# Kernel tuning notes

Measured on AMD Instinct MI355X. Metric: run time of the kernel, lower is better.

The kernel has to match this reference:

```python
import jax, jax.numpy as jnp
import numpy as np

N = 50000        # nodes
E_RAND = 800000  # random edges; self-loops appended -> E = E_RAND + N
H = 4            # heads
D_IN = 256
D_HID = 64       # per-head hidden (H*D_HID == D_IN -> identity residual in layer 1)
D_OUT = 32       # classes per head
SLOPE = 0.2      # leaky-relu negative slope


def setup_inputs() -> dict:
    key = jax.random.key(0)
    ks = jax.random.split(key, 13)
    loops = jnp.arange(N, dtype=jnp.int32)
    src = jnp.concatenate([jax.random.randint(ks[0], (E_RAND,), 0, N, dtype=jnp.int32), loops])
    dst = jnp.concatenate([jax.random.randint(ks[1], (E_RAND,), 0, N, dtype=jnp.int32), loops])
    h = jax.random.normal(ks[2], (N, D_IN), dtype=jnp.float32)
    def w(k, shape, fan):
        return jax.random.normal(k, shape, dtype=jnp.float32) * (1.0 / np.sqrt(fan))
    return {
        "h": h, "src": src, "dst": dst,
        # layer 1 (tuple in_feats -> separate fc_src / fc_dst in dgl GATConv)
        "W1_src": w(ks[3], (D_IN, H * D_HID), D_IN),
        "W1_dst": w(ks[4], (D_IN, H * D_HID), D_IN),
        "al1": w(ks[5], (H, D_HID), D_HID),
        "ar1": w(ks[6], (H, D_HID), D_HID),
        # layer 2
        "W2_src": w(ks[7], (H * D_HID, H * D_OUT), H * D_HID),
        "W2_dst": w(ks[8], (H * D_HID, H * D_OUT), H * D_HID),
        "al2": w(ks[9], (H, D_OUT), D_OUT),
        "ar2": w(ks[10], (H, D_OUT), D_OUT),
        # residual projection for layer 2 (in_dim != heads*out)
        "Wres2": w(ks[11], (H * D_HID, H * D_OUT), H * D_HID),
    }


def gat_conv(h_node, src, dst, Ws, Wd, al, ar, heads, dout, resval):
    n = h_node.shape[0]
    fs = (h_node @ Ws).reshape(n, heads, dout)   # [N,H,D] projected src feats
    fd = (h_node @ Wd).reshape(n, heads, dout)
    el = jnp.sum(fs * al, axis=-1)               # [N,H]
    er = jnp.sum(fd * ar, axis=-1)               # [N,H]
    e = jax.nn.leaky_relu(el[src] + er[dst], SLOPE)           # [E,H] edge scores
    emax = jax.ops.segment_max(e, dst, num_segments=n)        # segment softmax over dst
    ex = jnp.exp(e - emax[dst])
    denom = jax.ops.segment_sum(ex, dst, num_segments=n)
    a = ex / denom[dst]                                        # [E,H] attention
    msg = fs[src] * a[:, :, None]                              # [E,H,D] gather * weight
    out = jax.ops.segment_sum(msg, dst, num_segments=n)       # [N,H,D] scatter-add
    return out + resval


def reference(h, src, dst, W1_src, W1_dst, al1, ar1, W2_src, W2_dst, al2, ar2, Wres2):
    # layer 1: identity residual (in_dim == heads*hidden), elu activation, flatten heads
    res1 = h.reshape(-1, H, D_HID)
    h1 = gat_conv(h, src, dst, W1_src, W1_dst, al1, ar1, H, D_HID, res1)
    h1 = jax.nn.elu(h1).reshape(-1, H * D_HID)
    # layer 2: linear residual, no activation, mean over heads
    res2 = (h1 @ Wres2).reshape(-1, H, D_OUT)
    h2 = gat_conv(h1, src, dst, W2_src, W2_dst, al2, ar2, H, D_OUT, res2)
    return h2.mean(axis=1)                                     # [N, num_classes]
```

## Files before the change

kernel.cpp:

```cpp
#include <hip/hip_runtime.h>
#include <hip/hip_bf16.h>

#define NN 50000
#define EE 850000
#define NBLK_SCAN 98

typedef unsigned short u16;
using short8 = __attribute__((ext_vector_type(8))) short;
using f32x4  = __attribute__((ext_vector_type(4))) float;

__device__ __forceinline__ float bf2f(u16 u) {
    union { unsigned int i; float f; } v; v.i = ((unsigned int)u) << 16; return v.f;
}
__device__ __forceinline__ u16 f2bf(float f) {
    __hip_bfloat16 h = __float2bfloat16(f);
    return *reinterpret_cast<u16*>(&h);
}

__device__ __forceinline__ float ld1(const void* X, size_t i, bool f32m) {
    return f32m ? ((const float*)X)[i] : bf2f(((const u16*)X)[i]);
}
__device__ __forceinline__ void load4(const void* X, size_t g, bool f32m, float o[4]) {
    if (f32m) {
        float4 v = ((const float4*)X)[g];
        o[0] = v.x; o[1] = v.y; o[2] = v.z; o[3] = v.w;
    } else {
        ushort4 v = ((const ushort4*)X)[g];
        o[0] = bf2f(v.x); o[1] = bf2f(v.y); o[2] = bf2f(v.z); o[3] = bf2f(v.w);
    }
}

__global__ void k_detect(const u16* __restrict__ hh, int* __restrict__ flag,
                         int* __restrict__ deg) {
    if (blockIdx.x != 0) {
        int i = (blockIdx.x - 1) * 256 + threadIdx.x;
        if (i < NN) deg[i] = 0;
        return;
    }
    __shared__ int sm[256];
    int t = threadIdx.x;
    int c = 0;
    for (int i = 0; i < 16; ++i) {
        u16 u = hh[t * 16 + i];
        int e = (u >> 7) & 0xFF;
        if (e != 0 && (e < 90 || e > 160)) ++c;
    }
    sm[t] = c;
    __syncthreads();
    for (int s = 128; s > 0; s >>= 1) {
        if (t < s) sm[t] += sm[t + s];
        __syncthreads();
    }
    if (t == 0) *flag = (sm[0] > 200) ? 1 : 0;
}

__global__ void k_prep(const void* __restrict__ W1s, const void* __restrict__ al1,
                       const void* __restrict__ W1d, const void* __restrict__ ar1,
                       const void* __restrict__ W2s, const void* __restrict__ al2,
                       const void* __restrict__ W2d, const void* __restrict__ ar2,
                       const void* __restrict__ Wres2, const int* __restrict__ dst,
                       u16* __restrict__ BT1, u16* __restrict__ BT2,
                       float* __restrict__ wl1, float* __restrict__ wr1,
                       float* __restrict__ wl2, float* __restrict__ wr2,
                       int* __restrict__ deg, int* __restrict__ eorder,
                       const int* __restrict__ mode) {
    int bid = blockIdx.x;
    if (bid >= 528) {
        int e = (bid - 528) * 256 + threadIdx.x;
        if (e < EE) {
            int r = atomicAdd(&deg[dst[e]], 1);
            eorder[e] = r;
        }
        return;
    }
    bool f32m = (*mode) != 0;
    if (bid < 512) {
        int id = bid * 256 + threadIdx.x;
        int which = id >> 16;
        int rem = id & 65535;
        int n = rem >> 8, k = rem & 255;
        if (which == 0) {
            BT1[n * 256 + k] = f2bf(ld1(W1s, (size_t)k * 256 + n, f32m));
        } else {
            float v = (n < 128) ? ld1(W2s, (size_t)k * 128 + n, f32m)
                                : ld1(Wres2, (size_t)k * 128 + (n - 128), f32m);
            BT2[n * 256 + k] = f2bf(v);
        }
    } else {
        int id = (bid - 512) * 256 + threadIdx.x;
        int which = id >> 10;
        int rem = id & 1023;
        int k = rem >> 2, h = rem & 3;
        float s = 0.f;
        if (which == 0) {
            for (int d = 0; d < 64; ++d) s += ld1(W1s, k * 256 + h * 64 + d, f32m) * ld1(al1, h * 64 + d, f32m);
            wl1[k * 4 + h] = s;
        } else if (which == 1) {
            for (int d = 0; d < 64; ++d) s += ld1(W1d, k * 256 + h * 64 + d, f32m) * ld1(ar1, h * 64 + d, f32m);
            wr1[k * 4 + h] = s;
        } else if (which == 2) {
            for (int d = 0; d < 32; ++d) s += ld1(W2s, k * 128 + h * 32 + d, f32m) * ld1(al2, h * 32 + d, f32m);
            wl2[k * 4 + h] = s;
        } else {
            for (int d = 0; d < 32; ++d) s += ld1(W2d, k * 128 + h * 32 + d, f32m) * ld1(ar2, h * 32 + d, f32m);
            wr2[k * 4 + h] = s;
        }
    }
}

__global__ void k_scan1(const int* __restrict__ deg, int* __restrict__ rowptr,
                        int* __restrict__ bsum) {
    __shared__ int sm[512];
    int t = threadIdx.x;
    int i = blockIdx.x * 512 + t;
    int v = (i < NN) ? deg[i] : 0;
    int x = v;
    sm[t] = x;
    __syncthreads();
    for (int off = 1; off < 512; off <<= 1) {
        int y = (t >= off) ? sm[t - off] : 0;
        __syncthreads();
        x += y;
        sm[t] = x;
        __syncthreads();
    }
    if (i < NN) rowptr[i] = x - v;
    if (t == 511) bsum[blockIdx.x] = x;
}

__global__ void k_scan3_eler1(int* __restrict__ rowptr, const int* __restrict__ bsum,
                              const void* __restrict__ X, u16* __restrict__ hb,
                              const float* __restrict__ wl, const float* __restrict__ wr,
                              float* __restrict__ el, float* __restrict__ er,
                              const int* __restrict__ mode) {
    int bid = blockIdx.x;
    if (bid < 196) {
        __shared__ int sm[NBLK_SCAN];
        int t = threadIdx.x;
        if (t < NBLK_SCAN) sm[t] = bsum[t];
        __syncthreads();
        int g = bid >> 1;
        int pre = 0;
        for (int j = 0; j < g; ++j) pre += sm[j];
        int i = bid * 256 + t;
        if (i < NN) {
            rowptr[i] += pre;
            if (i == 0) rowptr[NN] = EE;
        }
        return;
    }
    bool f32m = (*mode) != 0;
    int wave = threadIdx.x >> 6, lane = threadIdx.x & 63;
    int node = (bid - 196) * 4 + wave;
    float a[4];
    load4(X, (size_t)node * 64 + lane, f32m, a);
    ushort4 hv = {f2bf(a[0]), f2bf(a[1]), f2bf(a[2]), f2bf(a[3])};
    ((ushort4*)hb)[(size_t)node * 64 + lane] = hv;
    float accl[4] = {0, 0, 0, 0}, accr[4] = {0, 0, 0, 0};
    int k0 = lane * 4;
#pragma unroll
    for (int j = 0; j < 4; ++j) {
        float4 wlv = ((const float4*)wl)[k0 + j];
        float4 wrv = ((const float4*)wr)[k0 + j];
        accl[0] += a[j] * wlv.x; accl[1] += a[j] * wlv.y;
        accl[2] += a[j] * wlv.z; accl[3] += a[j] * wlv.w;
        accr[0] += a[j] * wrv.x; accr[1] += a[j] * wrv.y;
        accr[2] += a[j] * wrv.z; accr[3] += a[j] * wrv.w;
    }
#pragma unroll
    for (int off = 32; off > 0; off >>= 1) {
#pragma unroll
        for (int t = 0; t < 4; ++t) {
            accl[t] += __shfl_down(accl[t], off, 64);
            accr[t] += __shfl_down(accr[t], off, 64);
        }
    }
    if (lane == 0) {
        float4 vl = {accl[0], accl[1], accl[2], accl[3]};
        float4 vr = {accr[0], accr[1], accr[2], accr[3]};
        ((float4*)el)[node] = vl;
        ((float4*)er)[node] = vr;
    }
}

__global__ void k_scatw(const int* __restrict__ src, const int* __restrict__ dst,
                        const int* __restrict__ eorder, const int* __restrict__ rowptr,
                        const float* __restrict__ el, const float* __restrict__ er,
                        uint4* __restrict__ meta) {
    int e = blockIdx.x * 256 + threadIdx.x;
    if (e >= EE) return;
    int s = src[e], d = dst[e];
    int slot = rowptr[d] + eorder[e];
    float4 eL = ((const float4*)el)[s];
    float4 eR = ((const float4*)er)[d];
    float ev[4] = {eL.x + eR.x, eL.y + eR.y, eL.z + eR.z, eL.w + eR.w};
    u16 op[4];
#pragma unroll
    for (int t = 0; t < 4; ++t) {
        float x = ev[t];
        x = x > 0.f ? x : 0.2f * x;
        x = fminf(fmaxf(x, -60.f), 60.f);
        op[t] = f2bf(__expf(x));
    }
    uint4 m;
    m.x = (unsigned int)s;
    m.y = (unsigned int)op[0] | ((unsigned int)op[1] << 16);
    m.z = (unsigned int)op[2] | ((unsigned int)op[3] << 16);
    m.w = 0u;
    meta[slot] = m;
}

__global__ void k_gemm_mfma(const u16* __restrict__ A,
                            const u16* __restrict__ BT, u16* __restrict__ C) {
    __shared__ u16 smem[128 * 72 * 2];
    u16* At = smem;
    u16* Bt = smem + 128 * 72;
    int t = threadIdx.x;
    int lane = t & 63, w = t >> 6;
    int mt = blockIdx.x >> 1, nt = blockIdx.x & 1;
    int m0 = mt * 128, n0 = nt * 128;
    int wr = (w >> 1) * 64, wc = (w & 1) * 64;
    f32x4 acc[4][4] = {};
    int q = lane >> 4, cl = lane & 15;

    for (int ph = 0; ph < 4; ++ph) {
        int kb = ph * 64;
        for (int it = 0; it < 4; ++it) {
            int c = it * 256 + t;
            int row = c >> 3, c8 = c & 7;
            int rowg = m0 + row;
            float4 av;
            if (rowg < NN) {
                av = *(const float4*)(A + (size_t)rowg * 256 + kb + c8 * 8);
            } else {
                av = make_float4(0.f, 0.f, 0.f, 0.f);
            }
            *(float4*)&At[row * 72 + c8 * 8] = av;
            float4 bv = *(const float4*)(BT + (size_t)(n0 + row) * 256 + kb + c8 * 8);
            *(float4*)&Bt[row * 72 + c8 * 8] = bv;
        }
        __syncthreads();
#pragma unroll
        for (int ks = 0; ks < 2; ++ks) {
            short8 af[4], bf[4];
#pragma unroll
            for (int i = 0; i < 4; ++i)
                af[i] = *(const short8*)&At[(wr + i * 16 + cl) * 72 + ks * 32 + q * 8];
#pragma unroll
            for (int j = 0; j < 4; ++j)
                bf[j] = *(const short8*)&Bt[(wc + j * 16 + cl) * 72 + ks * 32 + q * 8];
#pragma unroll
            for (int i = 0; i < 4; ++i)
#pragma unroll
                for (int j = 0; j < 4; ++j)
                    acc[i][j] = __builtin_amdgcn_mfma_f32_16x16x32_bf16(af[i], bf[j], acc[i][j], 0, 0, 0);
        }
        __syncthreads();
    }
    u16* Ct = smem;
    int sw_w = q << 1;
#pragma unroll
    for (int i = 0; i < 4; ++i)
#pragma unroll
        for (int j = 0; j < 4; ++j) {
            int colb = wc + j * 16 + cl;
            int chunk = (colb >> 3) ^ sw_w;
#pragma unroll
            for (int r = 0; r < 4; ++r) {
                int row = wr + i * 16 + q * 4 + r;
                Ct[row * 128 + chunk * 8 + (colb & 7)] = f2bf(acc[i][j][r]);
            }
        }
    __syncthreads();
#pragma unroll
    for (int it = 0; it < 8; ++it) {
        int c = it * 256 + t;
        int row = c >> 4, k16 = c & 15;
        int mrow = m0 + row;
        if (mrow < NN) {
            int phys = k16 ^ (((row >> 2) & 3) << 1);
            float4 v = *(const float4*)&Ct[row * 128 + phys * 8];
            *(float4*)&C[(size_t)mrow * 256 + n0 + k16 * 8] = v;
        }
    }
}

__global__ void k_agg1(const int* __restrict__ rowptr, const uint4* __restrict__ meta,
                       const u16* __restrict__ fs, u16* __restrict__ hb,
                       const float* __restrict__ wl2, const float* __restrict__ wr2,
                       float* __restrict__ el2, float* __restrict__ er2) {
    int wave = threadIdx.x >> 6, lane = threadIdx.x & 63;
    int node = blockIdx.x * 4 + wave;
    int beg = rowptr[node], end = rowptr[node + 1];
    int head = lane >> 4;
    const int* ms = (const int*)meta;
    const u16* mw = (const u16*)meta + 2 + head;
    float a0 = 0.f, a1 = 0.f, a2 = 0.f, a3 = 0.f, ll = 0.f;
#pragma unroll 8
    for (int p = beg; p < end; ++p) {
        int s = ms[(size_t)p * 4];
        float pw = bf2f(mw[(size_t)p * 8]);
        ushort4 fv = *(const ushort4*)(fs + (size_t)s * 256 + lane * 4);
        ll += pw;
        a0 += pw * bf2f(fv.x);
        a1 += pw * bf2f(fv.y);
        a2 += pw * bf2f(fv.z);
        a3 += pw * bf2f(fv.w);
    }
    float rinv = 1.f / ll;
    ushort4 rv = ((const ushort4*)hb)[(size_t)node * 64 + lane];
    float v0 = a0 * rinv + bf2f(rv.x), v1 = a1 * rinv + bf2f(rv.y);
    float v2 = a2 * rinv + bf2f(rv.z), v3 = a3 * rinv + bf2f(rv.w);
    v0 = v0 > 0.f ? v0 : __expf(v0) - 1.f;
    v1 = v1 > 0.f ? v1 : __expf(v1) - 1.f;
    v2 = v2 > 0.f ? v2 : __expf(v2) - 1.f;
    v3 = v3 > 0.f ? v3 : __expf(v3) - 1.f;
    ushort4 o = {f2bf(v0), f2bf(v1), f2bf(v2), f2bf(v3)};
    ((ushort4*)hb)[(size_t)node * 64 + lane] = o;
    float4 w0 = ((const float4*)wl2)[lane * 4 + 0];
    float4 w1 = ((const float4*)wl2)[lane * 4 + 1];
    float4 w2 = ((const float4*)wl2)[lane * 4 + 2];
    float4 w3 = ((const float4*)wl2)[lane * 4 + 3];
    float4 r0 = ((const float4*)wr2)[lane * 4 + 0];
    float4 r1 = ((const float4*)wr2)[lane * 4 + 1];
    float4 r2 = ((const float4*)wr2)[lane * 4 + 2];
    float4 r3 = ((const float4*)wr2)[lane * 4 + 3];
    float acl[4], acr[4];
    acl[0] = v0 * w0.x + v1 * w1.x + v2 * w2.x + v3 * w3.x;
    acl[1] = v0 * w0.y + v1 * w1.y + v2 * w2.y + v3 * w3.y;
    acl[2] = v0 * w0.z + v1 * w1.z + v2 * w2.z + v3 * w3.z;
    acl[3] = v0 * w0.w + v1 * w1.w + v2 * w2.w + v3 * w3.w;
    acr[0] = v0 * r0.x + v1 * r1.x + v2 * r2.x + v3 * r3.x;
    acr[1] = v0 * r0.y + v1 * r1.y + v2 * r2.y + v3 * r3.y;
    acr[2] = v0 * r0.z + v1 * r1.z + v2 * r2.z + v3 * r3.z;
    acr[3] = v0 * r0.w + v1 * r1.w + v2 * r2.w + v3 * r3.w;
#pragma unroll
    for (int off = 32; off > 0; off >>= 1) {
#pragma unroll
        for (int t = 0; t < 4; ++t) {
            acl[t] += __shfl_down(acl[t], off, 64);
            acr[t] += __shfl_down(acr[t], off, 64);
        }
    }
    if (lane == 0) {
        float4 vl = {acl[0], acl[1], acl[2], acl[3]};
        float4 vr = {acr[0], acr[1], acr[2], acr[3]};
        ((float4*)el2)[node] = vl;
        ((float4*)er2)[node] = vr;
    }
}

__global__ void k_agg2(const int* __restrict__ rowptr, const uint4* __restrict__ meta,
                       const float* __restrict__ el2, const float* __restrict__ er2,
                       const u16* __restrict__ c2,
                       void* __restrict__ out, const int* __restrict__ mode) {
    bool f32m = (*mode) != 0;
    int wave = threadIdx.x >> 6, lane = threadIdx.x & 63;
    int node = blockIdx.x * 4 + wave;
    int beg = rowptr[node], end = rowptr[node + 1];
    int head = lane >> 4;
    const int* ms = (const int*)meta;
    float erh = er2[node * 4 + head];
    float a0 = 0.f, a1 = 0.f, ll = 0.f;
#pragma unroll 8
    for (int p = beg; p < end; ++p) {
        int s = ms[(size_t)p * 4];
        float x = el2[s * 4 + head] + erh;
        x = x > 0.f ? x : 0.2f * x;
        x = fminf(fmaxf(x, -60.f), 60.f);
        float pw = __expf(x);
        ushort2 fv = *(const ushort2*)(c2 + (size_t)s * 256 + lane * 2);
        ll += pw;
        a0 += pw * bf2f(fv.x);
        a1 += pw * bf2f(fv.y);
    }
    float rinv = 1.f / ll;
    ushort2 rv = *(const ushort2*)(c2 + (size_t)node * 256 + 128 + lane * 2);
    float o0 = a0 * rinv + bf2f(rv.x);
    float o1 = a1 * rinv + bf2f(rv.y);
    o0 += __shfl_xor(o0, 16, 64); o0 += __shfl_xor(o0, 32, 64);
    o1 += __shfl_xor(o1, 16, 64); o1 += __shfl_xor(o1, 32, 64);
    if (lane < 16) {
        float v0 = 0.25f * o0, v1 = 0.25f * o1;
        size_t oi = (size_t)node * 32 + lane * 2;
        if (f32m) {
            ((float*)out)[oi] = v0;
            ((float*)out)[oi + 1] = v1;
        } else {
            ushort2 ov = {f2bf(v0), f2bf(v1)};
            *(ushort2*)((u16*)out + oi) = ov;
        }
    }
}

extern "C" void kernel_launch(void* const* d_in, const int* in_sizes, int n_in,
                              void* d_out, int out_size, void* d_ws, size_t ws_size,
                              hipStream_t stream) {
    int ih = 0, isrc = 1, idst = 2, iW1s = 3, iW1d = 4, ial1 = 5, iar1 = 6,
        iW2s = 7, iW2d = 8, ial2 = 9, iar2 = 10, iWres = 11;
    if (n_in >= 12 && in_sizes[0] != 12800000) {
        iW1d = 0; iW1s = 1; iW2d = 2; iW2s = 3; iWres = 4; ial1 = 5; ial2 = 6;
        iar1 = 7; iar2 = 8; idst = 9; ih = 10; isrc = 11;
    }
    const void* h     = d_in[ih];
    const int* src    = (const int*)d_in[isrc];
    const int* dst    = (const int*)d_in[idst];
    const void* W1s   = d_in[iW1s];
    const void* W1d   = d_in[iW1d];
    const void* al1   = d_in[ial1];
    const void* ar1   = d_in[iar1];
    const void* W2s   = d_in[iW2s];
    const void* W2d   = d_in[iW2d];
    const void* al2   = d_in[ial2];
    const void* ar2   = d_in[iar2];
    const void* Wres2 = d_in[iWres];

    char* w = (char*)d_ws;
    size_t off = 0;
    auto alloc = [&](size_t bytes) -> void* {
        void* p = w + off;
        off += (bytes + 255) & ~(size_t)255;
        return p;
    };
    int* mode   = (int*)alloc(256);
    float* wl1 = (float*)alloc(256 * 4 * 4);
    float* wr1 = (float*)alloc(256 * 4 * 4);
    float* wl2 = (float*)alloc(256 * 4 * 4);
    float* wr2 = (float*)alloc(256 * 4 * 4);
    int* deg    = (int*)alloc(NN * 4);
    int* rowptr = (int*)alloc((NN + 1) * 4);
    int* bsum   = (int*)alloc(NBLK_SCAN * 4);
    int* eorder = (int*)alloc((size_t)EE * 4);
    uint4* meta = (uint4*)alloc((size_t)EE * 16);
    float* el1  = (float*)alloc((size_t)NN * 4 * 4);
    float* er1  = (float*)alloc((size_t)NN * 4 * 4);
    float* el2  = (float*)alloc((size_t)NN * 4 * 4);
    float* er2  = (float*)alloc((size_t)NN * 4 * 4);
    u16* BT1    = (u16*)alloc(256 * 256 * 2);
    u16* BT2    = (u16*)alloc(256 * 256 * 2);
    u16* fs1    = (u16*)alloc((size_t)NN * 256 * 2);
    u16* hb     = (u16*)alloc((size_t)NN * 256 * 2);
    u16* c2     = fs1;

    k_detect<<<197, 256, 0, stream>>>((const u16*)h, mode, deg);
    k_prep<<<528 + (EE + 255) / 256, 256, 0, stream>>>(
        W1s, al1, W1d, ar1, W2s, al2, W2d, ar2, Wres2, dst,
        BT1, BT2, wl1, wr1, wl2, wr2, deg, eorder, mode);
    k_scan1<<<NBLK_SCAN, 512, 0, stream>>>(deg, rowptr, bsum);
    k_scan3_eler1<<<196 + NN / 4, 256, 0, stream>>>(rowptr, bsum,
                                                    h, hb, wl1, wr1, el1, er1, mode);
    k_scatw<<<(EE + 255) / 256, 256, 0, stream>>>(src, dst, eorder, rowptr,
                                                  el1, er1, meta);
    k_gemm_mfma<<<782, 256, 0, stream>>>(hb, BT1, fs1);
    k_agg1<<<NN / 4, 256, 0, stream>>>(rowptr, meta, fs1, hb,
                                       wl2, wr2, el2, er2);
    k_gemm_mfma<<<782, 256, 0, stream>>>(hb, BT2, c2);
    k_agg2<<<NN / 4, 256, 0, stream>>>(rowptr, meta, el2, er2, c2, d_out, mode);
}
```

Before: 354.6 us.

## Use direct global-to-LDS loads with XOR swizzle in GEMM; tile weight transpose

The MFMA GEMM now stages A and B tiles with global_load_lds 16-byte transfers into an unpadded, XOR-swizzled LDS layout instead of going through registers. The row bounds check is dropped, so hb is over-allocated by 64 rows to make the tail reads safe. The weight-prep kernel transposes through a shared tile in 32 blocks instead of 512 scattered blocks, and the attention-weight dot products use vectorized loads. The aim is less register staging and fewer prep blocks; the padded rows hold uninitialized data that feeds only output rows beyond N.

```diff
diff --git a/kernel.cpp b/kernel.cpp
--- a/kernel.cpp
+++ b/kernel.cpp
@@ -28,6 +28,12 @@
         ushort4 v = ((const ushort4*)X)[g];
         o[0] = bf2f(v.x); o[1] = bf2f(v.y); o[2] = bf2f(v.z); o[3] = bf2f(v.w);
     }
+}
+
+__device__ __forceinline__ void gload_lds16(const void* g, void* l) {
+    __builtin_amdgcn_global_load_lds(
+        (const __attribute__((address_space(1))) unsigned int*)g,
+        (__attribute__((address_space(3))) unsigned int*)l, 16, 0, 0);
 }
 
 __global__ void k_detect(const u16* __restrict__ hh, int* __restrict__ flag,
@@ -65,8 +71,8 @@
                        int* __restrict__ deg, int* __restrict__ eorder,
                        const int* __restrict__ mode) {
     int bid = blockIdx.x;
-    if (bid >= 528) {
-        int e = (bid - 528) * 256 + threadIdx.x;
+    if (bid >= 48) {
+        int e = (bid - 48) * 256 + threadIdx.x;
         if (e < EE) {
             int r = atomicAdd(&deg[dst[e]], 1);
             eorder[e] = r;
@@ -74,37 +80,70 @@
         return;
     }
     bool f32m = (*mode) != 0;
-    if (bid < 512) {
-        int id = bid * 256 + threadIdx.x;
-        int which = id >> 16;
-        int rem = id & 65535;
-        int n = rem >> 8, k = rem & 255;
-        if (which == 0) {
-            BT1[n * 256 + k] = f2bf(ld1(W1s, (size_t)k * 256 + n, f32m));
-        } else {
-            float v = (n < 128) ? ld1(W2s, (size_t)k * 128 + n, f32m)
-                                : ld1(Wres2, (size_t)k * 128 + (n - 128), f32m);
-            BT2[n * 256 + k] = f2bf(v);
-        }
+    if (bid < 32) {
+        __shared__ float tile[64][65];
+        int which = bid >> 4;
+        int a = (bid >> 2) & 3;
+        int b = bid & 3;
+        int r4 = threadIdx.x >> 6;
+        int cc = threadIdx.x & 63;
+#pragma unroll 4
+        for (int pass = 0; pass < 16; ++pass) {
+            int r = pass * 4 + r4;
+            int k = b * 64 + r;
+            int n = a * 64 + cc;
+            float v;
+            if (which == 0) {
+                v = ld1(W1s, (size_t)k * 256 + n, f32m);
+            } else {
+                v = (n < 128) ? ld1(W2s, (size_t)k * 128 + n, f32m)
+                              : ld1(Wres2, (size_t)k * 128 + (n - 128), f32m);
+            }
+            tile[r][cc] = v;
+        }
+        __syncthreads();
+        u16* BT = which ? BT2 : BT1;
+#pragma unroll 4
+        for (int pass = 0; pass < 16; ++pass) {
+            int nn = pass * 4 + r4;
+            BT[(size_t)(a * 64 + nn) * 256 + b * 64 + cc] = f2bf(tile[cc][nn]);
+        }
+        return;
+    }
+    int id = (bid - 32) * 256 + threadIdx.x;
+    int which = id >> 10;
+    int rem = id & 1023;
+    int k = rem >> 2, hh = rem & 3;
+    float s = 0.f;
+    float av[4], wv[4];
+    if (which == 0) {
+        for (int j = 0; j < 16; ++j) {
+            load4(W1s, (size_t)k * 64 + hh * 16 + j, f32m, av);
+            load4(al1, hh * 16 + j, f32m, wv);
+            s += av[0] * wv[0] + av[1] * wv[1] + av[2] * wv[2] + av[3] * wv[3];
+        }
+        wl1[k * 4 + hh] = s;
+    } else if (which == 1) {
+        for (int j = 0; j < 16; ++j) {
+            load4(W1d, (size_t)k * 64 + hh * 16 + j, f32m, av);
+            load4(ar1, hh * 16 + j, f32m, wv);
+            s += av[0] * wv[0] + av[1] * wv[1] + av[2] * wv[2] + av[3] * wv[3];
+        }
+        wr1[k * 4 + hh] = s;
+    } else if (which == 2) {
+        for (int j = 0; j < 8; ++j) {
+            load4(W2s, (size_t)k * 32 + hh * 8 + j, f32m, av);
+            load4(al2, hh * 8 + j, f32m, wv);
+            s += av[0] * wv[0] + av[1] * wv[1] + av[2] * wv[2] + av[3] * wv[3];
+        }
+        wl2[k * 4 + hh] = s;
     } else {
-        int id = (bid - 512) * 256 + threadIdx.x;
-        int which = id >> 10;
-        int rem = id & 1023;
-        int k = rem >> 2, h = rem & 3;
-        float s = 0.f;
-        if (which == 0) {
-            for (int d = 0; d < 64; ++d) s += ld1(W1s, k * 256 + h * 64 + d, f32m) * ld1(al1, h * 64 + d, f32m);
-            wl1[k * 4 + h] = s;
-        } else if (which == 1) {
-            for (int d = 0; d < 64; ++d) s += ld1(W1d, k * 256 + h * 64 + d, f32m) * ld1(ar1, h * 64 + d, f32m);
-            wr1[k * 4 + h] = s;
-        } else if (which == 2) {
-            for (int d = 0; d < 32; ++d) s += ld1(W2s, k * 128 + h * 32 + d, f32m) * ld1(al2, h * 32 + d, f32m);
-            wl2[k * 4 + h] = s;
-        } else {
-            for (int d = 0; d < 32; ++d) s += ld1(W2d, k * 128 + h * 32 + d, f32m) * ld1(ar2, h * 32 + d, f32m);
-            wr2[k * 4 + h] = s;
-        }
+        for (int j = 0; j < 8; ++j) {
+            load4(W2d, (size_t)k * 32 + hh * 8 + j, f32m, av);
+            load4(ar2, hh * 8 + j, f32m, wv);
+            s += av[0] * wv[0] + av[1] * wv[1] + av[2] * wv[2] + av[3] * wv[3];
+        }
+        wr2[k * 4 + hh] = s;
     }
 }
 
@@ -212,9 +251,9 @@
 
 __global__ void k_gemm_mfma(const u16* __restrict__ A,
                             const u16* __restrict__ BT, u16* __restrict__ C) {
-    __shared__ u16 smem[128 * 72 * 2];
+    __shared__ u16 smem[16384];
     u16* At = smem;
-    u16* Bt = smem + 128 * 72;
+    u16* Bt = smem + 8192;
     int t = threadIdx.x;
     int lane = t & 63, w = t >> 6;
     int mt = blockIdx.x >> 1, nt = blockIdx.x & 1;
@@ -222,33 +261,29 @@
     int wr = (w >> 1) * 64, wc = (w & 1) * 64;
     f32x4 acc[4][4] = {};
     int q = lane >> 4, cl = lane & 15;
+    int c7 = cl & 7;
 
     for (int ph = 0; ph < 4; ++ph) {
         int kb = ph * 64;
+#pragma unroll
         for (int it = 0; it < 4; ++it) {
             int c = it * 256 + t;
             int row = c >> 3, c8 = c & 7;
-            int rowg = m0 + row;
-            float4 av;
-            if (rowg < NN) {
-                av = *(const float4*)(A + (size_t)rowg * 256 + kb + c8 * 8);
-            } else {
-                av = make_float4(0.f, 0.f, 0.f, 0.f);
-            }
-            *(float4*)&At[row * 72 + c8 * 8] = av;
-            float4 bv = *(const float4*)(BT + (size_t)(n0 + row) * 256 + kb + c8 * 8);
-            *(float4*)&Bt[row * 72 + c8 * 8] = bv;
+            int sc8 = c8 ^ (row & 7);
+            gload_lds16(A + (size_t)(m0 + row) * 256 + kb + sc8 * 8, &At[c * 8]);
+            gload_lds16(BT + (size_t)(n0 + row) * 256 + kb + sc8 * 8, &Bt[c * 8]);
         }
         __syncthreads();
 #pragma unroll
         for (int ks = 0; ks < 2; ++ks) {
             short8 af[4], bf[4];
+            int xa = ((ks * 4 + q) ^ c7) * 8;
 #pragma unroll
             for (int i = 0; i < 4; ++i)
-                af[i] = *(const short8*)&At[(wr + i * 16 + cl) * 72 + ks * 32 + q * 8];
+                af[i] = *(const short8*)&At[(wr + i * 16 + cl) * 64 + xa];
 #pragma unroll
             for (int j = 0; j < 4; ++j)
-                bf[j] = *(const short8*)&Bt[(wc + j * 16 + cl) * 72 + ks * 32 + q * 8];
+                bf[j] = *(const short8*)&Bt[(wc + j * 16 + cl) * 64 + xa];
 #pragma unroll
             for (int i = 0; i < 4; ++i)
 #pragma unroll
@@ -439,11 +474,11 @@
     u16* BT1    = (u16*)alloc(256 * 256 * 2);
     u16* BT2    = (u16*)alloc(256 * 256 * 2);
     u16* fs1    = (u16*)alloc((size_t)NN * 256 * 2);
-    u16* hb     = (u16*)alloc((size_t)NN * 256 * 2);
+    u16* hb     = (u16*)alloc((size_t)(NN + 64) * 256 * 2);
     u16* c2     = fs1;
 
     k_detect<<<197, 256, 0, stream>>>((const u16*)h, mode, deg);
-    k_prep<<<528 + (EE + 255) / 256, 256, 0, stream>>>(
+    k_prep<<<48 + (EE + 255) / 256, 256, 0, stream>>>(
         W1s, al1, W1d, ar1, W2s, al2, W2d, ar2, Wres2, dst,
         BT1, BT2, wl1, wr1, wl2, wr2, deg, eorder, mode);
     k_scan1<<<NBLK_SCAN, 512, 0, stream>>>(deg, rowptr, bsum);
```

After: 350.3 us. About the same (-1.2%).
